# Optimization experiments

Measured on AMD Instinct MI355X. Metric: run time of the kernel, lower is better.

The kernel has to match this reference:

```python
import jax, jax.numpy as jnp
import numpy as np

K = 5  # kernel_size per dim
# 2^dim = 4 active degree-1 B-spline products per edge (dim=2)
BITS = jnp.array([[0, 0], [1, 0], [0, 1], [1, 1]], dtype=jnp.int32)  # [S,2]


def spline_basis(edge_attr):
    """Open B-spline basis, degree=1, dim=2, kernel_size=5 per dim.
    Returns basis weights [E,S] and flattened kernel indices [E,S]."""
    v = edge_attr * (K - 1)                 # scale pseudo-coords to knot grid
    i0 = jnp.floor(v)
    f = v - i0                              # fractional part, [E,2]
    # per-dim linear weights: f for bit=1, (1-f) for bit=0
    w = jnp.where(BITS[None] == 1, f[:, None, :], 1.0 - f[:, None, :])  # [E,S,2]
    basis = w[..., 0] * w[..., 1]           # [E,S]
    idx = jnp.minimum(i0.astype(jnp.int32)[:, None, :] + BITS[None], K - 1)  # [E,S,2]
    kidx = idx[..., 0] + K * idx[..., 1]    # flatten 2D kernel index -> [0,25)
    return basis, kidx


def spline_conv(x, src, dst, basis, kidx, W, root, bias, n):
    # transform-then-gather: y[n,k,:] = x[n] @ W[k]
    y = jnp.einsum('ni,kio->nko', x, W)                 # [N,25,out]
    g = y[src[:, None], kidx]                           # gather [E,S,out]
    msg = jnp.einsum('es,eso->eo', basis, g)            # weighted sum over S
    agg = jax.ops.segment_sum(msg, dst, num_segments=n)  # scatter-add to targets
    return agg + x @ root + bias                        # root weight + bias


def setup_inputs() -> dict:
    key = jax.random.key(0)
    ks = jax.random.split(key, 8)
    N, E, IN, H, OUT = 50000, 400000, 32, 64, 64
    x = jax.random.normal(ks[0], (N, IN), jnp.float32)
    edge_index = jax.random.randint(ks[1], (2, E), 0, N, dtype=jnp.int32)
    edge_attr = jax.random.uniform(ks[2], (E, 2), jnp.float32)

    def glorot(k, shape):
        fan = shape[-2] + shape[-1]
        return jax.random.normal(k, shape, jnp.float32) * jnp.sqrt(2.0 / fan)

    W1 = glorot(ks[3], (K * K, IN, H));  root1 = glorot(ks[4], (IN, H));  b1 = jnp.zeros((H,), jnp.float32)
    W2 = glorot(ks[5], (K * K, H, OUT)); root2 = glorot(ks[6], (H, OUT)); b2 = jnp.zeros((OUT,), jnp.float32)
    fc_w = glorot(ks[7], (OUT, 3));      fc_b = jnp.zeros((3,), jnp.float32)
    return dict(x=x, edge_index=edge_index, edge_attr=edge_attr,
                W1=W1, root1=root1, b1=b1, W2=W2, root2=root2, b2=b2,
                fc_w=fc_w, fc_b=fc_b)


def reference(x, edge_index, edge_attr, W1, root1, b1, W2, root2, b2, fc_w, fc_b):
    # eval-mode forward (dropout is identity at inference)
    n = x.shape[0]
    src, dst = edge_index[0], edge_index[1]
    basis, kidx = spline_basis(edge_attr)
    h = jax.nn.relu(spline_conv(x, src, dst, basis, kidx, W1, root1, b1, n))
    h = jax.nn.relu(spline_conv(h, src, dst, basis, kidx, W2, root2, b2, n))
    return h @ fc_w + fc_b
```

## Files before the change

kernel.cpp:

```cpp
#include <hip/hip_runtime.h>
#include <stdint.h>

typedef __attribute__((ext_vector_type(8))) short short8;
typedef __attribute__((ext_vector_type(4))) float f32x4;
typedef __attribute__((ext_vector_type(4))) unsigned short ushort4v;

__device__ __forceinline__ unsigned short f2bf(float f) {
    unsigned int u = __float_as_uint(f);
    u = (u + 0x7FFFu + ((u >> 16) & 1u)) >> 16;
    return (unsigned short)u;
}
__device__ __forceinline__ float bf2f(unsigned short h) {
    return __uint_as_float(((unsigned int)h) << 16);
}
__device__ __forceinline__ int cell_of(float ax, float ay) {
    int c0 = (int)floorf(ax * 4.f); c0 = min(max(c0, 0), 3);
    int c1 = (int)floorf(ay * 4.f); c1 = min(max(c1, 0), 3);
    return c0 + 4 * c1;
}

__global__ __launch_bounds__(256) void zero_kernel(int* __restrict__ p, int n) {
    int t = blockIdx.x * 256 + threadIdx.x;
    if (t < n) p[t] = 0;
}

template<int KIN>
__device__ __forceinline__ void pack_cell_elem(const float* __restrict__ W,
                                               unsigned short* __restrict__ pkc, int u) {
    constexpr int KCH = KIN / 8;
    if (u >= 16 * 4 * KCH * 512) return;
    int low9 = u & 511;
    int grp  = u >> 9;
    int kc = grp % KCH; grp /= KCH;
    int c  = grp & 3;
    int cell = grp >> 2;
    int lane = low9 >> 3, j = low9 & 7;
    int k = kc * 32 + (lane >> 4) * 8 + j;
    int t = k / KIN, i = k % KIN;
    int k0 = (cell & 3) + (t & 1);   if (k0 > 4) k0 = 4;
    int k1 = (cell >> 2) + (t >> 1); if (k1 > 4) k1 = 4;
    float val = W[((size_t)(k0 + 5 * k1) * KIN + i) * 64 + (c * 16 + (lane & 15))];
    pkc[u] = f2bf(val);
}

template<int KIN>
__device__ __forceinline__ void pack_root_elem(const float* __restrict__ root,
                                               unsigned short* __restrict__ pkr, int u) {
    constexpr int KCHr = KIN / 32;
    if (u >= 4 * KCHr * 512) return;
    int low9 = u & 511;
    int grp  = u >> 9;
    int lane = low9 >> 3, j = low9 & 7;
    int kc = grp % KCHr, c = grp / KCHr;
    int k = kc * 32 + (lane >> 4) * 8 + j;
    int o = c * 16 + (lane & 15);
    float v = root[(size_t)k * 64 + o];
    unsigned short h = f2bf(v);
    pkr[(size_t)(grp * 2) * 512 + low9]     = h;
    pkr[(size_t)(grp * 2 + 1) * 512 + low9] = f2bf(v - bf2f(h));
}

__global__ __launch_bounds__(256) void prep_kernel(
    const float* __restrict__ attr, const int* __restrict__ dst,
    int* __restrict__ hist, int* __restrict__ dhist, int E,
    const float* __restrict__ W1, const float* __restrict__ W2,
    const float* __restrict__ root1, const float* __restrict__ root2,
    unsigned short* __restrict__ pkc1, unsigned short* __restrict__ pkc2,
    unsigned short* __restrict__ pkr1, unsigned short* __restrict__ pkr2,
    const float* __restrict__ x, unsigned short* __restrict__ xb, int n4,
    int EB)
{
    __shared__ int wcnt[4][16];
    int b = blockIdx.x;
    if (b < EB) {
        int e = b * 256 + threadIdx.x;
        int lane = threadIdx.x & 63, wave = threadIdx.x >> 6;
        int cell = -1;
        if (e < E) {
            float2 a = reinterpret_cast<const float2*>(attr)[e];
            cell = cell_of(a.x, a.y);
            atomicAdd(&dhist[dst[e]], 1);
        }
        #pragma unroll
        for (int c = 0; c < 16; c++) {
            unsigned long long m = __ballot(cell == c);
            if (lane == 0) wcnt[wave][c] = __popcll(m);
        }
        __syncthreads();
        if (threadIdx.x < 16) {
            int c = threadIdx.x;
            int tot = wcnt[0][c] + wcnt[1][c] + wcnt[2][c] + wcnt[3][c];
            if (tot) atomicAdd(&hist[c], tot);
        }
        return;
    }
    b -= EB;
    if (b < 512)  { pack_cell_elem<32>(W1, pkc1, b * 256 + threadIdx.x); return; }
    b -= 512;
    if (b < 1024) { pack_cell_elem<64>(W2, pkc2, b * 256 + threadIdx.x); return; }
    b -= 1024;
    if (b < 8)    { pack_root_elem<32>(root1, pkr1, b * 256 + threadIdx.x); return; }
    b -= 8;
    if (b < 16)   { pack_root_elem<64>(root2, pkr2, b * 256 + threadIdx.x); return; }
    b -= 16;
    {
        int t = b * 256 + threadIdx.x;
        if (t < n4) {
            float4 v = reinterpret_cast<const float4*>(x)[t];
            ushort4v o = { f2bf(v.x), f2bf(v.y), f2bf(v.z), f2bf(v.w) };
            reinterpret_cast<ushort4v*>(xb)[t] = o;
        }
    }
}

__global__ __launch_bounds__(1024) void scanA_kernel(const int* __restrict__ dhist,
                                                     int* __restrict__ nof,
                                                     int* __restrict__ bsum, int Np1) {
    __shared__ int wsum[16];
    int tid = threadIdx.x, lane = tid & 63, w = tid >> 6;
    int i = blockIdx.x * 1024 + tid;
    int v = (i < Np1) ? dhist[i] : 0;
    int s = v;
    #pragma unroll
    for (int off = 1; off < 64; off <<= 1) {
        int t = __shfl_up(s, off);
        if (lane >= off) s += t;
    }
    if (lane == 63) wsum[w] = s;
    __syncthreads();
    if (tid == 0) {
        int a = 0;
        #pragma unroll
        for (int k = 0; k < 16; k++) { int t = wsum[k]; wsum[k] = a; a += t; }
        bsum[blockIdx.x] = a;
    }
    __syncthreads();
    if (i < Np1) nof[i] = wsum[w] + s - v;
}

__global__ void scan_small_kernel(const int* __restrict__ hist, int* __restrict__ off_e,
                                  int* __restrict__ off_b, int* __restrict__ cursor,
                                  const int* __restrict__ bsum, int* __restrict__ bbase, int NB) {
    if (threadIdx.x == 0 && blockIdx.x == 0) {
        int se = 0, sb = 0;
        for (int c = 0; c < 16; c++) {
            off_e[c] = se; off_b[c] = sb; cursor[c] = se;
            se += hist[c]; sb += (hist[c] + 63) >> 6;
        }
        off_e[16] = se; off_b[16] = sb;
        int a = 0;
        for (int bks = 0; bks < NB; bks++) { int t = bsum[bks]; bbase[bks] = a; a += t; }
    }
}

__global__ __launch_bounds__(256) void scatter_kernel(const float* __restrict__ attr,
                                                      const int* __restrict__ dst,
                                                      const int* __restrict__ nof,
                                                      const int* __restrict__ bbase,
                                                      int* __restrict__ bucket,
                                                      int* __restrict__ cursor,
                                                      int* __restrict__ dhist,
                                                      int* __restrict__ dstpos, int E) {
    __shared__ int wcnt[4][16];
    __shared__ int wbase[4][16];
    int e = blockIdx.x * 256 + threadIdx.x;
    int lane = threadIdx.x & 63, wave = threadIdx.x >> 6;
    int cell = -1;
    if (e < E) {
        float2 a = reinterpret_cast<const float2*>(attr)[e];
        cell = cell_of(a.x, a.y);
        int d = dst[e];
        int rank = atomicSub(&dhist[d], 1) - 1;
        dstpos[e] = nof[d] + bbase[d >> 10] + rank;
    }
    int myrank = 0;
    #pragma unroll
    for (int c = 0; c < 16; c++) {
        unsigned long long m = __ballot(cell == c);
        if (cell == c) myrank = __popcll(m & ((1ull << lane) - 1ull));
        if (lane == 0) wcnt[wave][c] = __popcll(m);
    }
    __syncthreads();
    if (threadIdx.x < 16) {
        int c = threadIdx.x;
        int t0 = wcnt[0][c], t1 = wcnt[1][c], t2 = wcnt[2][c], t3 = wcnt[3][c];
        int tot = t0 + t1 + t2 + t3;
        int g = tot ? atomicAdd(&cursor[c], tot) : 0;
        wbase[0][c] = g;
        wbase[1][c] = g + t0;
        wbase[2][c] = g + t0 + t1;
        wbase[3][c] = g + t0 + t1 + t2;
    }
    __syncthreads();
    if (e < E) bucket[wbase[wave][cell] + myrank] = e;
}

template<int KIN>
__global__ __launch_bounds__(256) void layer_kernel(
    const unsigned short* __restrict__ Xb,
    const unsigned short* __restrict__ pkr, float* __restrict__ rt,
    const float* __restrict__ bias, int N, int RG,
    const unsigned short* __restrict__ pkc, unsigned short* __restrict__ msg,
    const int* __restrict__ src, const float* __restrict__ attr,
    const int* __restrict__ bucket, const int* __restrict__ dstpos,
    const int* __restrict__ off_e, const int* __restrict__ off_b)
{
    constexpr int KCHr = KIN / 32;
    constexpr int KCH  = 4 * KCHr;
    __shared__ unsigned short Blds[4 * KCH * 512];

    const int lane = threadIdx.x & 63;
    const int wave = threadIdx.x >> 6;
    const int lrow = lane & 15, lch = lane >> 4;

    if (blockIdx.x < RG) {
        const int mbase = blockIdx.x * 64 + wave * 16;
        short8 afrag[KCHr];
        {
            int row = mbase + lrow;
            if (row > N - 1) row = N - 1;
            const unsigned short* ap = Xb + (size_t)row * KIN + lch * 8;
            #pragma unroll
            for (int kc = 0; kc < KCHr; kc++)
                afrag[kc] = *reinterpret_cast<const short8*>(ap + kc * 32);
        }
        f32x4 acc[4];
        #pragma unroll
        for (int c = 0; c < 4; c++) acc[c] = (f32x4){0.f, 0.f, 0.f, 0.f};
        #pragma unroll
        for (int c = 0; c < 4; c++) {
            #pragma unroll
            for (int kc = 0; kc < KCHr; kc++) {
                short8 bh = *reinterpret_cast<const short8*>(pkr + ((size_t)(c * KCHr + kc) * 2    ) * 512 + lane * 8);
                short8 bl = *reinterpret_cast<const short8*>(pkr + ((size_t)(c * KCHr + kc) * 2 + 1) * 512 + lane * 8);
                acc[c] = __builtin_amdgcn_mfma_f32_16x16x32_bf16(afrag[kc], bh, acc[c], 0, 0, 0);
                acc[c] = __builtin_amdgcn_mfma_f32_16x16x32_bf16(afrag[kc], bl, acc[c], 0, 0, 0);
            }
        }
        #pragma unroll
        for (int c = 0; c < 4; c++) {
            int o = c * 16 + lrow;
            float bv = bias[o];
            #pragma unroll
            for (int r = 0; r < 4; r++) {
                int m = mbase + lch * 4 + r;
                if (m < N) rt[(size_t)m * 64 + o] = acc[c][r] + bv;
            }
        }
        return;
    }

    const int b = blockIdx.x - RG;
    if (b >= off_b[16]) return;
    int cell = 0;
    #pragma unroll
    for (int c = 1; c < 16; c++) cell += (b >= off_b[c]);
    const int tile = b - off_b[cell];

    {
        const short8* sp = reinterpret_cast<const short8*>(pkc + (size_t)cell * (4 * KCH * 512));
        short8* dp = reinterpret_cast<short8*>(Blds);
        #pragma unroll
        for (int p = 0; p < (4 * KCH * 512 / 8) / 256; p++)
            dp[p * 256 + threadIdx.x] = sp[p * 256 + threadIdx.x];
    }

    const int ebeg = off_e[cell];
    const int eend = off_e[cell + 1];
    const int eslot = ebeg + (tile * 4 + wave) * 16 + lrow;
    const bool valid = eslot < eend;

    int eid = 0, s = 0, mp = -1;
    float ax = 0.f, ay = 0.f;
    if (valid) {
        eid = bucket[eslot];
        s = src[eid];
        mp = dstpos[eid];
        float2 a = reinterpret_cast<const float2*>(attr)[eid];
        ax = a.x; ay = a.y;
    }
    const float f0 = ax * 4.f - (float)(cell & 3);
    const float f1 = ay * 4.f - (float)(cell >> 2);
    float w[4] = { (1.f - f0) * (1.f - f1), f0 * (1.f - f1),
                   (1.f - f0) * f1,         f0 * f1 };

    short8 xfrag[KCHr];
    {
        const unsigned short* xp = Xb + (size_t)s * KIN + lch * 8;
        #pragma unroll
        for (int kcr = 0; kcr < KCHr; kcr++)
            xfrag[kcr] = *reinterpret_cast<const short8*>(xp + kcr * 32);
    }

    float wr[4][4];
    int pv[4];
    #pragma unroll
    for (int r = 0; r < 4; r++) {
        int er = lch * 4 + r;
        #pragma unroll
        for (int t = 0; t < 4; t++) wr[t][r] = __shfl(w[t], er);
        pv[r] = __shfl(mp, er);
    }

    __syncthreads();

    #pragma unroll
    for (int ch = 0; ch < 2; ch++) {
        f32x4 accT[4][2];
        #pragma unroll
        for (int t = 0; t < 4; t++)
            #pragma unroll
            for (int c2 = 0; c2 < 2; c2++)
                accT[t][c2] = (f32x4){0.f, 0.f, 0.f, 0.f};

        #pragma unroll
        for (int t = 0; t < 4; t++) {
            #pragma unroll
            for (int kcr = 0; kcr < KCHr; kcr++) {
                #pragma unroll
                for (int c2 = 0; c2 < 2; c2++) {
                    int c = ch * 2 + c2;
                    short8 bf = *reinterpret_cast<const short8*>(
                        &Blds[(size_t)((c * KCH) + (t * KCHr + kcr)) * 512 + lane * 8]);
                    accT[t][c2] = __builtin_amdgcn_mfma_f32_16x16x32_bf16(xfrag[kcr], bf, accT[t][c2], 0, 0, 0);
                }
            }
        }

        #pragma unroll
        for (int c2 = 0; c2 < 2; c2++) {
            const int o = (ch * 2 + c2) * 16 + lrow;
            #pragma unroll
            for (int r = 0; r < 4; r++) {
                if (pv[r] >= 0) {
                    float m = wr[0][r] * accT[0][c2][r] + wr[1][r] * accT[1][c2][r]
                            + wr[2][r] * accT[2][c2][r] + wr[3][r] * accT[3][c2][r];
                    msg[(size_t)pv[r] * 64 + o] = f2bf(m);
                }
            }
        }
    }
}

template<int MODE>
__global__ __launch_bounds__(256) void segsum_kernel(
    const unsigned short* __restrict__ msg, const float* __restrict__ rt,
    const int* __restrict__ nof, const int* __restrict__ bbase,
    unsigned short* __restrict__ hout,
    const float* __restrict__ fcw, const float* __restrict__ fcb,
    float* __restrict__ out, int N)
{
    int n = blockIdx.x * 4 + (threadIdx.x >> 6);
    if (n >= N) return;
    int lane = threadIdx.x & 63;
    float acc = rt[(size_t)n * 64 + lane];
    int jb = nof[n]     + bbase[n >> 10];
    int je = nof[n + 1] + bbase[(n + 1) >> 10];
    int j = jb;
    for (; j + 3 < je; j += 4) {
        float a0 = bf2f(msg[(size_t)(j + 0) * 64 + lane]);
        float a1 = bf2f(msg[(size_t)(j + 1) * 64 + lane]);
        float a2 = bf2f(msg[(size_t)(j + 2) * 64 + lane]);
        float a3 = bf2f(msg[(size_t)(j + 3) * 64 + lane]);
        acc += a0; acc += a1; acc += a2; acc += a3;
    }
    for (; j < je; j++) acc += bf2f(msg[(size_t)j * 64 + lane]);
    acc = fmaxf(acc, 0.f);
    if (MODE == 0) {
        hout[(size_t)n * 64 + lane] = f2bf(acc);
    } else {
        float p0 = acc * fcw[lane * 3 + 0];
        float p1 = acc * fcw[lane * 3 + 1];
        float p2 = acc * fcw[lane * 3 + 2];
        #pragma unroll
        for (int off = 32; off; off >>= 1) {
            p0 += __shfl_xor(p0, off);
            p1 += __shfl_xor(p1, off);
            p2 += __shfl_xor(p2, off);
        }
        if (lane == 0) {
            out[(size_t)n * 3 + 0] = p0 + fcb[0];
            out[(size_t)n * 3 + 1] = p1 + fcb[1];
            out[(size_t)n * 3 + 2] = p2 + fcb[2];
        }
    }
}

extern "C" void kernel_launch(void* const* d_in, const int* in_sizes, int n_in,
                              void* d_out, int out_size, void* d_ws, size_t ws_size,
                              hipStream_t stream)
{
    const float* x     = (const float*)d_in[0];
    const int*   ei    = (const int*)  d_in[1];
    const float* attr  = (const float*)d_in[2];
    const float* W1    = (const float*)d_in[3];
    const float* root1 = (const float*)d_in[4];
    const float* b1    = (const float*)d_in[5];
    const float* W2    = (const float*)d_in[6];
    const float* root2 = (const float*)d_in[7];
    const float* b2    = (const float*)d_in[8];
    const float* fcw   = (const float*)d_in[9];
    const float* fcb   = (const float*)d_in[10];

    const int N = in_sizes[0] / 32;
    const int E = in_sizes[1] / 2;
    const int* srcp = ei;
    const int* dstp = ei + E;

    char* wsp = (char*)d_ws;
    auto alloc = [&](size_t bytes) -> char* {
        char* p = wsp;
        wsp += (bytes + 255) & ~(size_t)255;
        return p;
    };
    const int NB = (N + 1 + 1023) / 1024;

    float*          rt       = (float*)alloc((size_t)N * 64 * 4);
    unsigned short* xb       = (unsigned short*)alloc((size_t)N * 32 * 2);
    unsigned short* h1b      = (unsigned short*)alloc((size_t)N * 64 * 2);
    unsigned short* pkr1     = (unsigned short*)alloc((size_t)4 * 1 * 2 * 512 * 2);
    unsigned short* pkr2     = (unsigned short*)alloc((size_t)4 * 2 * 2 * 512 * 2);
    unsigned short* pkc1     = (unsigned short*)alloc((size_t)16 * 4 * 4 * 512 * 2);
    unsigned short* pkc2     = (unsigned short*)alloc((size_t)16 * 4 * 8 * 512 * 2);
    int*            bucket   = (int*)alloc((size_t)E * 4);
    int*            dstpos   = (int*)alloc((size_t)E * 4);
    int*            nof      = (int*)alloc((size_t)(N + 1) * 4);
    int*            bsum     = (int*)alloc((size_t)NB * 4);
    int*            bbase    = (int*)alloc((size_t)NB * 4);
    int*            off_e    = (int*)alloc(17 * 4);
    int*            off_b    = (int*)alloc(17 * 4);
    int*            cursor   = (int*)alloc(16 * 4);
    int*            zbase    = (int*)alloc((size_t)(16 + N + 1) * 4);
    int*            hist     = zbase;
    int*            dhist    = zbase + 16;
    unsigned short* msg      = (unsigned short*)alloc((size_t)E * 64 * 2);

    const int ZN = 16 + N + 1;
    zero_kernel<<<(ZN + 255) / 256, 256, 0, stream>>>(zbase, ZN);

    const int EB = (E + 255) / 256;
    const int CB = (N * 8 + 255) / 256;
    const int prep_grid = EB + 512 + 1024 + 8 + 16 + CB;

    prep_kernel<<<prep_grid, 256, 0, stream>>>(attr, dstp, hist, dhist, E,
                                               W1, W2, root1, root2,
                                               pkc1, pkc2, pkr1, pkr2,
                                               x, xb, N * 8, EB);
    scanA_kernel<<<NB, 1024, 0, stream>>>(dhist, nof, bsum, N + 1);
    scan_small_kernel<<<1, 64, 0, stream>>>(hist, off_e, off_b, cursor, bsum, bbase, NB);
    scatter_kernel<<<EB, 256, 0, stream>>>(attr, dstp, nof, bbase, bucket, cursor, dhist, dstpos, E);

    const int RG = (N + 63) / 64;
    const int lgrid = RG + (E + 63) / 64 + 16;
    const int sgrid = (N + 3) / 4;

    layer_kernel<32><<<lgrid, 256, 0, stream>>>(xb, pkr1, rt, b1, N, RG,
                                                pkc1, msg, srcp, attr, bucket, dstpos, off_e, off_b);
    segsum_kernel<0><<<sgrid, 256, 0, stream>>>(msg, rt, nof, bbase, h1b, fcw, fcb, (float*)d_out, N);

    layer_kernel<64><<<lgrid, 256, 0, stream>>>(h1b, pkr2, rt, b2, N, RG,
                                                pkc2, msg, srcp, attr, bucket, dstpos, off_e, off_b);
    segsum_kernel<1><<<sgrid, 256, 0, stream>>>(msg, rt, nof, bbase, nullptr, fcw, fcb, (float*)d_out, N);
}
```

Measured before the change: 187.4 us.

## Pack per-edge metadata into bucketed int4 and read weights directly from global

The scatter kernel now writes src, destination position and the two attribute floats as one int4 per bucketed slot, so the layer kernels read one coalesced 16-byte record instead of chasing bucket->eid->src/dstpos/attr through several indirect loads. The layer kernels also stop staging the per-cell weight block into LDS and remove the block barrier, loading B fragments straight from global/L2. This cuts dependent random gathers in both layers but makes every wave read the weights from cache instead of shared memory, and it raises the scatter kernel's write traffic.

```diff
diff --git a/kernel.cpp b/kernel.cpp
--- a/kernel.cpp
+++ b/kernel.cpp
@@ -154,24 +154,27 @@
 }
 
 __global__ __launch_bounds__(256) void scatter_kernel(const float* __restrict__ attr,
+                                                      const int* __restrict__ src,
                                                       const int* __restrict__ dst,
                                                       const int* __restrict__ nof,
                                                       const int* __restrict__ bbase,
-                                                      int* __restrict__ bucket,
+                                                      int4* __restrict__ emeta,
                                                       int* __restrict__ cursor,
-                                                      int* __restrict__ dhist,
-                                                      int* __restrict__ dstpos, int E) {
+                                                      int* __restrict__ dhist, int E) {
     __shared__ int wcnt[4][16];
     __shared__ int wbase[4][16];
     int e = blockIdx.x * 256 + threadIdx.x;
     int lane = threadIdx.x & 63, wave = threadIdx.x >> 6;
     int cell = -1;
+    float2 a = {0.f, 0.f};
+    int mp = 0, sv = 0;
     if (e < E) {
-        float2 a = reinterpret_cast<const float2*>(attr)[e];
+        a = reinterpret_cast<const float2*>(attr)[e];
         cell = cell_of(a.x, a.y);
         int d = dst[e];
         int rank = atomicSub(&dhist[d], 1) - 1;
-        dstpos[e] = nof[d] + bbase[d >> 10] + rank;
+        mp = nof[d] + bbase[d >> 10] + rank;
+        sv = src[e];
     }
     int myrank = 0;
     #pragma unroll
@@ -192,7 +195,10 @@
         wbase[3][c] = g + t0 + t1 + t2;
     }
     __syncthreads();
-    if (e < E) bucket[wbase[wave][cell] + myrank] = e;
+    if (e < E) {
+        int slot = wbase[wave][cell] + myrank;
+        emeta[slot] = make_int4(sv, mp, __float_as_int(a.x), __float_as_int(a.y));
+    }
 }
 
 template<int KIN>
@@ -201,13 +207,11 @@
     const unsigned short* __restrict__ pkr, float* __restrict__ rt,
     const float* __restrict__ bias, int N, int RG,
     const unsigned short* __restrict__ pkc, unsigned short* __restrict__ msg,
-    const int* __restrict__ src, const float* __restrict__ attr,
-    const int* __restrict__ bucket, const int* __restrict__ dstpos,
+    const int4* __restrict__ emeta,
     const int* __restrict__ off_e, const int* __restrict__ off_b)
 {
     constexpr int KCHr = KIN / 32;
     constexpr int KCH  = 4 * KCHr;
-    __shared__ unsigned short Blds[4 * KCH * 512];
 
     const int lane = threadIdx.x & 63;
     const int wave = threadIdx.x >> 6;
@@ -257,28 +261,17 @@
     for (int c = 1; c < 16; c++) cell += (b >= off_b[c]);
     const int tile = b - off_b[cell];
 
-    {
-        const short8* sp = reinterpret_cast<const short8*>(pkc + (size_t)cell * (4 * KCH * 512));
-        short8* dp = reinterpret_cast<short8*>(Blds);
-        #pragma unroll
-        for (int p = 0; p < (4 * KCH * 512 / 8) / 256; p++)
-            dp[p * 256 + threadIdx.x] = sp[p * 256 + threadIdx.x];
-    }
-
     const int ebeg = off_e[cell];
     const int eend = off_e[cell + 1];
     const int eslot = ebeg + (tile * 4 + wave) * 16 + lrow;
     const bool valid = eslot < eend;
 
-    int eid = 0, s = 0, mp = -1;
-    float ax = 0.f, ay = 0.f;
-    if (valid) {
-        eid = bucket[eslot];
-        s = src[eid];
-        mp = dstpos[eid];
-        float2 a = reinterpret_cast<const float2*>(attr)[eid];
-        ax = a.x; ay = a.y;
-    }
+    const int4 em = emeta[valid ? eslot : ebeg];
+    const int s = em.x;
+    const int mp = valid ? em.y : -1;
+    const float ax = __int_as_float(em.z);
+    const float ay = __int_as_float(em.w);
+
     const float f0 = ax * 4.f - (float)(cell & 3);
     const float f1 = ay * 4.f - (float)(cell >> 2);
     float w[4] = { (1.f - f0) * (1.f - f1), f0 * (1.f - f1),
@@ -302,7 +295,7 @@
         pv[r] = __shfl(mp, er);
     }
 
-    __syncthreads();
+    const unsigned short* Bp = pkc + (size_t)cell * (4 * KCH * 512) + lane * 8;
 
     #pragma unroll
     for (int ch = 0; ch < 2; ch++) {
@@ -321,7 +314,7 @@
                 for (int c2 = 0; c2 < 2; c2++) {
                     int c = ch * 2 + c2;
                     short8 bf = *reinterpret_cast<const short8*>(
-                        &Blds[(size_t)((c * KCH) + (t * KCHr + kcr)) * 512 + lane * 8]);
+                        Bp + (size_t)((c * KCH) + (t * KCHr + kcr)) * 512);
                     accT[t][c2] = __builtin_amdgcn_mfma_f32_16x16x32_bf16(xfrag[kcr], bf, accT[t][c2], 0, 0, 0);
                 }
             }
@@ -422,8 +415,7 @@
     unsigned short* pkr2     = (unsigned short*)alloc((size_t)4 * 2 * 2 * 512 * 2);
     unsigned short* pkc1     = (unsigned short*)alloc((size_t)16 * 4 * 4 * 512 * 2);
     unsigned short* pkc2     = (unsigned short*)alloc((size_t)16 * 4 * 8 * 512 * 2);
-    int*            bucket   = (int*)alloc((size_t)E * 4);
-    int*            dstpos   = (int*)alloc((size_t)E * 4);
+    int4*           emeta    = (int4*)alloc((size_t)E * 16);
     int*            nof      = (int*)alloc((size_t)(N + 1) * 4);
     int*            bsum     = (int*)alloc((size_t)NB * 4);
     int*            bbase    = (int*)alloc((size_t)NB * 4);
@@ -448,17 +440,17 @@
                                                x, xb, N * 8, EB);
     scanA_kernel<<<NB, 1024, 0, stream>>>(dhist, nof, bsum, N + 1);
     scan_small_kernel<<<1, 64, 0, stream>>>(hist, off_e, off_b, cursor, bsum, bbase, NB);
-    scatter_kernel<<<EB, 256, 0, stream>>>(attr, dstp, nof, bbase, bucket, cursor, dhist, dstpos, E);
+    scatter_kernel<<<EB, 256, 0, stream>>>(attr, srcp, dstp, nof, bbase, emeta, cursor, dhist, E);
 
     const int RG = (N + 63) / 64;
     const int lgrid = RG + (E + 63) / 64 + 16;
     const int sgrid = (N + 3) / 4;
 
     layer_kernel<32><<<lgrid, 256, 0, stream>>>(xb, pkr1, rt, b1, N, RG,
-                                                pkc1, msg, srcp, attr, bucket, dstpos, off_e, off_b);
+                                                pkc1, msg, emeta, off_e, off_b);
     segsum_kernel<0><<<sgrid, 256, 0, stream>>>(msg, rt, nof, bbase, h1b, fcw, fcb, (float*)d_out, N);
 
     layer_kernel<64><<<lgrid, 256, 0, stream>>>(h1b, pkr2, rt, b2, N, RG,
-                                                pkc2, msg, srcp, attr, bucket, dstpos, off_e, off_b);
+                                                pkc2, msg, emeta, off_e, off_b);
     segsum_kernel<1><<<sgrid, 256, 0, stream>>>(msg, rt, nof, bbase, nullptr, fcw, fcb, (float*)d_out, N);
 }
```

Result: slower. 192.3 us (+2.6%).
